# Kernel tuning notes

Measured on AMD Instinct MI355X. Metric: run time of the kernel, lower is better.

The kernel has to match this reference:

```python
import jax, jax.numpy as jnp
import numpy as np

WS = 7       # window_size
NH = 4       # num_head = dim_in // dim_head
HD = 64      # dim_head
ALPHA = 0.1
BETA = 0.2
THETA = 0.5
EPS = 1e-5   # LayerNorm eps


def dwconv(x, w):
    # x: [b, C, h, w], w: [C, 1, k, k] depthwise, padding 'same', no bias
    return jax.lax.conv_general_dilated(
        x, w, window_strides=(1, 1), padding='SAME',
        feature_group_count=x.shape[1],
        dimension_numbers=('NCHW', 'OIHW', 'NCHW'))


def setup_inputs() -> dict:
    key = jax.random.key(0)
    ks = jax.random.split(key, 8)
    B, H, W, C = 32, 56, 56, 256
    s = 0.02
    return {
        'x': jax.random.normal(ks[0], (B, H, W, C), jnp.float32),
        'qkv_w': jax.random.normal(ks[1], (3 * C, C), jnp.float32) * s,
        'qkv_b': jnp.zeros((3 * C,), jnp.float32),
        'conv3_w': jax.random.normal(ks[2], (C, 1, 3, 3), jnp.float32) * s,
        'conv5_w': jax.random.normal(ks[3], (C, 1, 5, 5), jnp.float32) * s,
        'conv7_w': jax.random.normal(ks[4], (C, 1, 7, 7), jnp.float32) * s,
        'ffn_in_w': jax.random.normal(ks[5], (C, C), jnp.float32) * s,
        'ffn_out_w': jax.random.normal(ks[6], (C, C), jnp.float32) * s,
        'ln_g': jnp.ones((C,), jnp.float32),
        'ln_b': jnp.zeros((C,), jnp.float32),
    }


def reference(x, qkv_w, qkv_b, conv3_w, conv5_w, conv7_w, ffn_in_w, ffn_out_w, ln_g, ln_b):
    B, H, W, C = x.shape
    n1, n2 = H // WS, W // WS  # H,W divisible by WS -> no padding path
    # rearrange 'b (h1 n1) (w1 n2) c -> (b n1 n2) h1 w1 c' (window dim is MAJOR axis)
    xw = x.reshape(B, WS, n1, WS, n2, C).transpose(0, 2, 4, 1, 3, 5)
    xw = xw.reshape(B * n1 * n2, WS, WS, C)
    b, hw = B * n1 * n2, WS * WS

    shortcut = xw.reshape(b, hw, NH, HD).transpose(0, 2, 1, 3)  # [b, nh, hw, hd]
    qkv = xw.reshape(b, hw, C) @ qkv_w.T + qkv_b                # [b, hw, 3C]
    qkv = qkv.reshape(b, hw, 3, NH, HD).transpose(2, 0, 3, 1, 4)
    q, k, v = qkv[0], qkv[1], qkv[2]
    v = ALPHA * v + shortcut                                     # scaled residual into V
    shortcut2 = v.transpose(0, 2, 1, 3).reshape(b, WS, WS, C)    # [b, h, w, C]

    # SDPA with default scale hd^-0.5
    attn = jax.nn.softmax(jnp.einsum('bnqd,bnkd->bnqk', q, k) * (HD ** -0.5), axis=-1)
    x_spa = jnp.einsum('bnqk,bnkd->bnqd', attn, v)
    x_spa = x_spa.transpose(0, 2, 1, 3).reshape(b, WS, WS, C)

    # conv branches on modified v: v.transpose(-1,-2).reshape(b, C, h, w)
    xc = v.transpose(0, 1, 3, 2).reshape(b, C, WS, WS)
    c3 = dwconv(xc, conv3_w).transpose(0, 2, 3, 1)
    c5 = dwconv(xc, conv5_w).transpose(0, 2, 3, 1)
    c7 = dwconv(xc, conv7_w).transpose(0, 2, 3, 1)
    x_spa = 0.25 * (x_spa + c3 + c5 + c7)  # equal 0.25 branch weights

    xw = BETA * x_spa + shortcut2
    # inverse rearrange '(b n1 n2) h1 w1 c -> b (h1 n1) (w1 n2) c'
    xo = xw.reshape(B, n1, n2, WS, WS, C).transpose(0, 3, 1, 4, 2, 5).reshape(B, H, W, C)

    # FFN (bias=False) with scaled residual, then LayerNorm
    y = jax.nn.silu(xo @ ffn_in_w.T) @ ffn_out_w.T
    xo = THETA * y + xo
    mu = jnp.mean(xo, axis=-1, keepdims=True)
    var = jnp.var(xo, axis=-1, keepdims=True)
    return (xo - mu) / jnp.sqrt(var + EPS) * ln_g + ln_b
```

## Files before the change

### kernel.cpp

```cpp
#include <hip/hip_runtime.h>

typedef unsigned short u16;
typedef unsigned short u16x8 __attribute__((ext_vector_type(8)));
typedef unsigned short u16x4 __attribute__((ext_vector_type(4)));
typedef unsigned int   u32x2 __attribute__((ext_vector_type(2)));
typedef short          s16x8 __attribute__((ext_vector_type(8)));
typedef float          f32x4 __attribute__((ext_vector_type(4)));

#define DEV static __device__ __forceinline__

DEV float bf2f(u16 u){ unsigned int v = ((unsigned int)u) << 16; return __builtin_bit_cast(float, v); }
DEV u16 f2bf(float f){
  unsigned int u = __builtin_bit_cast(unsigned int, f);
  u += 0x7fffu + ((u >> 16) & 1u);
  return (u16)(u >> 16);
}

DEV f32x4 mfma16(u16x8 a, u16x8 b, f32x4 c){
  return __builtin_amdgcn_mfma_f32_16x16x32_bf16(
      __builtin_bit_cast(s16x8, a), __builtin_bit_cast(s16x8, b), c, 0, 0, 0);
}

DEV void g2l16(const void* g, void* l){
  __builtin_amdgcn_global_load_lds((const __attribute__((address_space(1))) void*)g,
                                   (__attribute__((address_space(3))) void*)l, 16, 0, 0);
}

DEV size_t xrow_from(int b, int hw){
  int h1 = hw / 7, w1 = hw - h1 * 7;
  return ((size_t)(((b >> 6) * 56 + h1 * 8 + ((b >> 3) & 7)) * 56 + (w1 * 8 + (b & 7)))) << 8;
}
DEV size_t xrow_off(int t){ int b = t / 49; return xrow_from(b, t - b * 49); }

__global__ __launch_bounds__(256) void k_prep(const float* __restrict__ qkvw,
                                              const float* __restrict__ c3,
                                              const float* __restrict__ c5,
                                              const float* __restrict__ c7,
                                              const float* __restrict__ fin,
                                              const float* __restrict__ fout,
                                              u16* __restrict__ wq, u16* __restrict__ wfi,
                                              u16* __restrict__ wfo, float* __restrict__ weffT){
  int id = blockIdx.x * 256 + threadIdx.x;
  if (id < 196608) { wq[id] = f2bf(qkvw[id]); return; }
  id -= 196608;
  if (id < 65536) { wfi[id] = f2bf(fin[id]); return; }
  id -= 65536;
  if (id < 65536) { wfo[id] = f2bf(fout[id]); return; }
  id -= 65536;
  if (id < 12544) {
    int c = id / 49, t = id - c * 49;
    int di = t / 7 - 3, dj = t % 7 - 3;
    float s = c7[c * 49 + t];
    if (di >= -2 && di <= 2 && dj >= -2 && dj <= 2) s += c5[c * 25 + (di + 2) * 5 + (dj + 2)];
    if (di >= -1 && di <= 1 && dj >= -1 && dj <= 1) s += c3[c * 9 + (di + 1) * 3 + (dj + 1)];
    weffT[c * 52 + t] = 0.05f * s;
  }
}

__global__ __launch_bounds__(256) void k_xbf(const float* __restrict__ x, u16* __restrict__ xbf){
  int tid = threadIdx.x;
  int tok = blockIdx.x * 4 + (tid >> 6);
  int c4 = (tid & 63) * 4;
  float4 v = *(const float4*)(x + xrow_off(tok) + c4);
  u16x4 o; o[0] = f2bf(v.x); o[1] = f2bf(v.y); o[2] = f2bf(v.z); o[3] = f2bf(v.w);
  *(u16x4*)&xbf[(size_t)tok * 256 + c4] = o;
}

__global__ __launch_bounds__(256) void k_qkv(const u16* __restrict__ xbf,
                                             const u16* __restrict__ wq,
                                             const float* __restrict__ qkvb,
                                             u16* __restrict__ qb, u16* __restrict__ kb,
                                             u16* __restrict__ vmb){
  __shared__ __align__(16) u16 As[128 * 64];
  __shared__ __align__(16) u16 Bs[128 * 64];
  const int bid = blockIdx.x;
  const int lin = (bid & 7) * 588 + (bid >> 3);
  const int bm = lin / 6, bn = lin - bm * 6;
  const int tid = threadIdx.x, lane = tid & 63, wid = tid >> 6;
  const int wm = wid >> 1, wn = wid & 1;
  const int r = lane & 15, g = lane >> 4;
  const int lr = lane >> 3;
  const int swz = ((lane & 7) ^ lr) * 16;
  const f32x4 fz = {0.f, 0.f, 0.f, 0.f};
  f32x4 acc[4][4];
#pragma unroll
  for (int m = 0; m < 4; ++m)
#pragma unroll
    for (int n = 0; n < 4; ++n) acc[m][n] = fz;

  const char* gA0 = (const char*)xbf + (size_t)bm * 128 * 512;
  const char* gB0 = (const char*)wq  + (size_t)bn * 128 * 512;

  for (int kt = 0; kt < 4; ++kt) {
#pragma unroll
    for (int ri = 0; ri < 4; ++ri) {
      int chunk = ri * 4 + wid;
      int row = chunk * 8 + lr;
      g2l16(gA0 + (size_t)row * 512 + kt * 128 + swz, (char*)As + chunk * 1024);
      g2l16(gB0 + (size_t)row * 512 + kt * 128 + swz, (char*)Bs + chunk * 1024);
    }
    __syncthreads();
#pragma unroll
    for (int kk = 0; kk < 2; ++kk) {
      u16x8 af[4], bq[4];
#pragma unroll
      for (int m = 0; m < 4; ++m)
        af[m] = *(const u16x8*)&As[(wm * 64 + m * 16 + r) * 64 + (((kk * 4 + g) ^ (r & 7)) * 8)];
#pragma unroll
      for (int n = 0; n < 4; ++n)
        bq[n] = *(const u16x8*)&Bs[(wn * 64 + n * 16 + r) * 64 + (((kk * 4 + g) ^ (r & 7)) * 8)];
#pragma unroll
      for (int m = 0; m < 4; ++m)
#pragma unroll
        for (int n = 0; n < 4; ++n) acc[m][n] = mfma16(af[m], bq[n], acc[m][n]);
    }
    __syncthreads();
  }

  const int sec = bn >> 1;
  const int cb = (bn & 1) * 128 + wn * 64;
  u16* const outp = (sec == 0) ? qb : (sec == 1) ? kb : vmb;
  float bias[4];
#pragma unroll
  for (int n = 0; n < 4; ++n) bias[n] = qkvb[sec * 256 + cb + n * 16 + r];
#pragma unroll
  for (int m = 0; m < 4; ++m) {
#pragma unroll
    for (int i = 0; i < 4; ++i) {
      int t = bm * 128 + wm * 64 + m * 16 + g * 4 + i;
      u16* dst = outp + (size_t)t * 256 + cb;
      if (sec == 0) {
#pragma unroll
        for (int n = 0; n < 4; ++n) dst[n * 16 + r] = f2bf((acc[m][n][i] + bias[n]) * 0.125f);
      } else if (sec == 1) {
#pragma unroll
        for (int n = 0; n < 4; ++n) dst[n * 16 + r] = f2bf(acc[m][n][i] + bias[n]);
      } else {
        const u16* xsrc = xbf + (size_t)t * 256 + cb;
#pragma unroll
        for (int n = 0; n < 4; ++n)
          dst[n * 16 + r] = f2bf(0.1f * (acc[m][n][i] + bias[n]) + bf2f(xsrc[n * 16 + r]));
      }
    }
  }
}

template<int HW0, int NPIX>
DEV void conv_do(const float (&in_f)[49], const float (&wreg)[49], const u16* xs,
                 int c, size_t obase, u16* __restrict__ xo){
#pragma unroll
  for (int p = 0; p < NPIX; ++p) {
    const int hw = HW0 + p;
    const int i0 = hw / 7, j0 = hw % 7;
    float a = 0.f;
#pragma unroll
    for (int di = -3; di <= 3; ++di) {
      const int ii = i0 + di;
      if (ii < 0 || ii > 6) continue;
#pragma unroll
      for (int dj = -3; dj <= 3; ++dj) {
        const int jj = j0 + dj;
        if (jj < 0 || jj > 6) continue;
        a += in_f[ii * 7 + jj] * wreg[(di + 3) * 7 + (dj + 3)];
      }
    }
    float xsv = bf2f(xs[hw * 72 + c]);
    float outv = in_f[hw] + 0.05f * xsv + a;
    xo[obase + (size_t)hw * 256] = f2bf(outv);
  }
}

__global__ __launch_bounds__(256) void k_attn(const u16* __restrict__ qb,
                                              const u16* __restrict__ kb,
                                              const u16* __restrict__ vmb,
                                              const float* __restrict__ weffT,
                                              u16* __restrict__ xo){
  __shared__ __align__(16) u16 smem[18432];
  const int bx = blockIdx.x;
  const int b = bx >> 1, hp = bx & 1;
  const int tid = threadIdx.x, lane = tid & 63, wid = tid >> 6;
  const int hl = wid >> 1, hf = wid & 1;
  const int hg = hp * 2 + hl;
  const int vto = hl * 9216, po = hl * 9216 + 4608;
  const int r = lane & 15, g = lane >> 4;
  const size_t tok0 = (size_t)b * 49;
  const int hc = hg * 64;

  if (hf == 0) {
    int c = lane;
    u16 pix[49];
#pragma unroll
    for (int hw = 0; hw < 49; ++hw) pix[hw] = vmb[(tok0 + hw) * 256 + hc + c];
#pragma unroll
    for (int t2 = 0; t2 < 12; ++t2) {
      u32x2 w;
      w[0] = (unsigned)pix[4 * t2] | ((unsigned)pix[4 * t2 + 1] << 16);
      w[1] = (unsigned)pix[4 * t2 + 2] | ((unsigned)pix[4 * t2 + 3] << 16);
      *(u32x2*)&smem[vto + c * 72 + 4 * t2] = w;
    }
    u32x2 wl; wl[0] = (unsigned)pix[48]; wl[1] = 0u;
    *(u32x2*)&smem[vto + c * 72 + 48] = wl;
    u32x2 z; z[0] = 0u; z[1] = 0u;
    *(u32x2*)&smem[vto + c * 72 + 52] = z;
    *(u32x2*)&smem[vto + c * 72 + 56] = z;
    *(u32x2*)&smem[vto + c * 72 + 60] = z;
  }

  const int mt0 = hf * 2;
  const f32x4 fz = {0.f, 0.f, 0.f, 0.f};
  f32x4 s[2][4];
#pragma unroll
  for (int m = 0; m < 2; ++m)
#pragma unroll
    for (int n = 0; n < 4; ++n) s[m][n] = fz;
  u16x8 aq[2][2], bk[4][2];
#pragma unroll
  for (int m = 0; m < 2; ++m) {
    int qrow = (mt0 + m) * 16 + r; if (qrow > 48) qrow = 48;
    const u16* src = qb + (tok0 + qrow) * 256 + hc;
    aq[m][0] = *(const u16x8*)(src + g * 8);
    aq[m][1] = *(const u16x8*)(src + 32 + g * 8);
  }
#pragma unroll
  for (int n = 0; n < 4; ++n) {
    int krow = n * 16 + r; if (krow > 48) krow = 0;
    const u16* src = kb + (tok0 + krow) * 256 + hc;
    bk[n][0] = *(const u16x8*)(src + g * 8);
    bk[n][1] = *(const u16x8*)(src + 32 + g * 8);
  }
#pragma unroll
  for (int kk = 0; kk < 2; ++kk)
#pragma unroll
    for (int m = 0; m < 2; ++m)
#pragma unroll
      for (int n = 0; n < 4; ++n) s[m][n] = mfma16(aq[m][kk], bk[n][kk], s[m][n]);

#pragma unroll
  for (int m = 0; m < 2; ++m) {
#pragma unroll
    for (int i = 0; i < 4; ++i) {
      float x0 = s[m][0][i], x1 = s[m][1][i], x2 = s[m][2][i];
      float x3 = (r >= 1) ? -1e30f : s[m][3][i];
      float mx = fmaxf(fmaxf(x0, x1), fmaxf(x2, x3));
#pragma unroll
      for (int off = 1; off < 16; off <<= 1) mx = fmaxf(mx, __shfl_xor(mx, off, 64));
      float e0 = __expf(x0 - mx), e1 = __expf(x1 - mx), e2 = __expf(x2 - mx);
      float e3 = (r >= 1) ? 0.f : __expf(x3 - mx);
      float sum = e0 + e1 + e2 + e3;
#pragma unroll
      for (int off = 1; off < 16; off <<= 1) sum += __shfl_xor(sum, off, 64);
      float inv = 1.f / sum;
      int rowp = po + ((mt0 + m) * 16 + g * 4 + i) * 72;
      smem[rowp + r]       = f2bf(e0 * inv);
      smem[rowp + 16 + r]  = f2bf(e1 * inv);
      smem[rowp + 32 + r]  = f2bf(e2 * inv);
      smem[rowp + 48 + r]  = f2bf(e3 * inv);
    }
  }
  __syncthreads();

  f32x4 o[2][4];
#pragma unroll
  for (int m = 0; m < 2; ++m)
#pragma unroll
    for (int n = 0; n < 4; ++n) o[m][n] = fz;
#pragma unroll
  for (int kk = 0; kk < 2; ++kk) {
    u16x8 pa[2], vb[4];
#pragma unroll
    for (int m = 0; m < 2; ++m) pa[m] = *(const u16x8*)&smem[po + ((mt0 + m) * 16 + r) * 72 + kk * 32 + g * 8];
#pragma unroll
    for (int n = 0; n < 4; ++n) vb[n] = *(const u16x8*)&smem[vto + (n * 16 + r) * 72 + kk * 32 + g * 8];
#pragma unroll
    for (int m = 0; m < 2; ++m)
#pragma unroll
      for (int n = 0; n < 4; ++n) o[m][n] = mfma16(pa[m], vb[n], o[m][n]);
  }
#pragma unroll
  for (int m = 0; m < 2; ++m)
#pragma unroll
    for (int n = 0; n < 4; ++n)
#pragma unroll
      for (int i = 0; i < 4; ++i)
        smem[po + ((mt0 + m) * 16 + g * 4 + i) * 72 + n * 16 + r] = f2bf(o[m][n][i]);
  __syncthreads();

  {
    int c = lane;
    float in_f[49];
#pragma unroll
    for (int t2 = 0; t2 < 6; ++t2) {
      u16x8 raw = *(const u16x8*)&smem[vto + c * 72 + t2 * 8];
#pragma unroll
      for (int e = 0; e < 8; ++e) in_f[t2 * 8 + e] = bf2f(raw[e]);
    }
    in_f[48] = bf2f(smem[vto + c * 72 + 48]);
    float wreg[49];
    const float* wsrc = weffT + (size_t)(hc + c) * 52;
#pragma unroll
    for (int j = 0; j < 12; ++j) {
      float4 v = *(const float4*)(wsrc + j * 4);
      wreg[j * 4] = v.x; wreg[j * 4 + 1] = v.y; wreg[j * 4 + 2] = v.z; wreg[j * 4 + 3] = v.w;
    }
    wreg[48] = wsrc[48];
    size_t obase = tok0 * 256 + hc + c;
    if (hf == 0) conv_do<0, 25>(in_f, wreg, &smem[po], c, obase, xo);
    else         conv_do<25, 24>(in_f, wreg, &smem[po], c, obase, xo);
  }
}

__global__ __launch_bounds__(256) void k_ffn1(const u16* __restrict__ xo,
                                              const u16* __restrict__ wfi,
                                              u16* __restrict__ h){
  __shared__ __align__(16) u16 As[128 * 64];
  __shared__ __align__(16) u16 Bs[128 * 64];
  const int bid = blockIdx.x;
  const int lin = (bid & 7) * 196 + (bid >> 3);
  const int bm = lin >> 1, bn = lin & 1;
  const int tid = threadIdx.x, lane = tid & 63, wid = tid >> 6;
  const int wm = wid >> 1, wn = wid & 1;
  const int r = lane & 15, g = lane >> 4;
  const int lr = lane >> 3;
  const int swz = ((lane & 7) ^ lr) * 16;
  const f32x4 fz = {0.f, 0.f, 0.f, 0.f};
  f32x4 acc[4][4];
#pragma unroll
  for (int m = 0; m < 4; ++m)
#pragma unroll
    for (int n = 0; n < 4; ++n) acc[m][n] = fz;

  const char* gA0 = (const char*)xo + (size_t)bm * 128 * 512;
  const char* gB0 = (const char*)wfi + (size_t)bn * 128 * 512;

  for (int kt = 0; kt < 4; ++kt) {
#pragma unroll
    for (int ri = 0; ri < 4; ++ri) {
      int chunk = ri * 4 + wid;
      int row = chunk * 8 + lr;
      g2l16(gA0 + (size_t)row * 512 + kt * 128 + swz, (char*)As + chunk * 1024);
      g2l16(gB0 + (size_t)row * 512 + kt * 128 + swz, (char*)Bs + chunk * 1024);
    }
    __syncthreads();
#pragma unroll
    for (int kk = 0; kk < 2; ++kk) {
      u16x8 af[4], bq[4];
#pragma unroll
      for (int m = 0; m < 4; ++m)
        af[m] = *(const u16x8*)&As[(wm * 64 + m * 16 + r) * 64 + (((kk * 4 + g) ^ (r & 7)) * 8)];
#pragma unroll
      for (int n = 0; n < 4; ++n)
        bq[n] = *(const u16x8*)&Bs[(wn * 64 + n * 16 + r) * 64 + (((kk * 4 + g) ^ (r & 7)) * 8)];
#pragma unroll
      for (int m = 0; m < 4; ++m)
#pragma unroll
        for (int n = 0; n < 4; ++n) acc[m][n] = mfma16(af[m], bq[n], acc[m][n]);
    }
    __syncthreads();
  }
#pragma unroll
  for (int m = 0; m < 4; ++m)
#pragma unroll
    for (int i = 0; i < 4; ++i) {
      int t = bm * 128 + wm * 64 + m * 16 + g * 4 + i;
      u16* dst = h + (size_t)t * 256 + bn * 128 + wn * 64;
#pragma unroll
      for (int n = 0; n < 4; ++n) {
        float v = acc[m][n][i];
        float sg = v / (1.f + __expf(-v));
        dst[n * 16 + r] = f2bf(sg);
      }
    }
}

__global__ __launch_bounds__(512) void k_ffn2(const u16* __restrict__ h,
                                              const u16* __restrict__ wfo,
                                              const u16* __restrict__ xo,
                                              const float* __restrict__ lng,
                                              const float* __restrict__ lnb,
                                              float* __restrict__ out){
  __shared__ __align__(16) u16 As[128 * 64];
  __shared__ __align__(16) u16 Bs[256 * 64];
  __shared__ float red1[4][128];
  __shared__ float red2[4][128];
  const int bm = blockIdx.x;
  const int tid = threadIdx.x, lane = tid & 63, wid = tid >> 6;
  const int wm = wid >> 2, wn = wid & 3;
  const int r = lane & 15, g = lane >> 4;
  const int lr = lane >> 3;
  const int swz = ((lane & 7) ^ lr) * 16;
  const f32x4 fz = {0.f, 0.f, 0.f, 0.f};
  f32x4 acc[4][4];
#pragma unroll
  for (int m = 0; m < 4; ++m)
#pragma unroll
    for (int n = 0; n < 4; ++n) acc[m][n] = fz;

  for (int kt = 0; kt < 4; ++kt) {
#pragma unroll
    for (int ri = 0; ri < 2; ++ri) {
      int chunk = ri * 8 + wid;
      int row = chunk * 8 + lr;
      g2l16((const char*)h + (size_t)(bm * 128 + row) * 512 + kt * 128 + swz, (char*)As + chunk * 1024);
    }
#pragma unroll
    for (int ri = 0; ri < 4; ++ri) {
      int chunk = ri * 8 + wid;
      int row = chunk * 8 + lr;
      g2l16((const char*)wfo + (size_t)row * 512 + kt * 128 + swz, (char*)Bs + chunk * 1024);
    }
    __syncthreads();
#pragma unroll
    for (int kk = 0; kk < 2; ++kk) {
      u16x8 af[4], bq[4];
#pragma unroll
      for (int m = 0; m < 4; ++m)
        af[m] = *(const u16x8*)&As[(wm * 64 + m * 16 + r) * 64 + (((kk * 4 + g) ^ (r & 7)) * 8)];
#pragma unroll
      for (int n = 0; n < 4; ++n)
        bq[n] = *(const u16x8*)&Bs[(wn * 64 + n * 16 + r) * 64 + (((kk * 4 + g) ^ (r & 7)) * 8)];
#pragma unroll
      for (int m = 0; m < 4; ++m)
#pragma unroll
        for (int n = 0; n < 4; ++n) acc[m][n] = mfma16(af[m], bq[n], acc[m][n]);
    }
    __syncthreads();
  }

  float lg[4], lb[4];
#pragma unroll
  for (int n = 0; n < 4; ++n) {
    int col = wn * 64 + n * 16 + r;
    lg[n] = lng[col]; lb[n] = lnb[col];
  }
#pragma unroll
  for (int m = 0; m < 4; ++m)
#pragma unroll
    for (int i = 0; i < 4; ++i) {
      int t = bm * 128 + wm * 64 + m * 16 + g * 4 + i;
      const u16* xsrc = xo + (size_t)t * 256;
#pragma unroll
      for (int n = 0; n < 4; ++n) {
        int col = wn * 64 + n * 16 + r;
        acc[m][n][i] = 0.5f * acc[m][n][i] + bf2f(xsrc[col]);
      }
    }
#pragma unroll
  for (int m = 0; m < 4; ++m)
#pragma unroll
    for (int i = 0; i < 4; ++i) {
      float s1 = 0.f, s2 = 0.f;
#pragma unroll
      for (int n = 0; n < 4; ++n) { float v = acc[m][n][i]; s1 += v; s2 += v * v; }
#pragma unroll
      for (int off = 1; off < 16; off <<= 1) { s1 += __shfl_xor(s1, off, 64); s2 += __shfl_xor(s2, off, 64); }
      if (r == 0) {
        int rl = wm * 64 + m * 16 + g * 4 + i;
        red1[wn][rl] = s1; red2[wn][rl] = s2;
      }
    }
  __syncthreads();
#pragma unroll
  for (int m = 0; m < 4; ++m)
#pragma unroll
    for (int i = 0; i < 4; ++i) {
      int rl = wm * 64 + m * 16 + g * 4 + i;
      float S1 = red1[0][rl] + red1[1][rl] + red1[2][rl] + red1[3][rl];
      float S2 = red2[0][rl] + red2[1][rl] + red2[2][rl] + red2[3][rl];
      float mu = S1 * (1.f / 256.f);
      float var = S2 * (1.f / 256.f) - mu * mu;
      float rstd = rsqrtf(var + 1e-5f);
      int t = bm * 128 + rl;
      int b49 = t / 49, hw = t - b49 * 49;
      size_t ob = xrow_from(b49, hw);
#pragma unroll
      for (int n = 0; n < 4; ++n) {
        int col = wn * 64 + n * 16 + r;
        out[ob + col] = (acc[m][n][i] - mu) * rstd * lg[n] + lb[n];
      }
    }
}

extern "C" void kernel_launch(void* const* d_in, const int* in_sizes, int n_in,
                              void* d_out, int out_size, void* d_ws, size_t ws_size,
                              hipStream_t stream) {
  (void)in_sizes; (void)n_in; (void)out_size; (void)ws_size;
  const float* x     = (const float*)d_in[0];
  const float* qkvw  = (const float*)d_in[1];
  const float* qkvb  = (const float*)d_in[2];
  const float* c3    = (const float*)d_in[3];
  const float* c5    = (const float*)d_in[4];
  const float* c7    = (const float*)d_in[5];
  const float* fin   = (const float*)d_in[6];
  const float* fout  = (const float*)d_in[7];
  const float* lng   = (const float*)d_in[8];
  const float* lnb   = (const float*)d_in[9];
  float* out = (float*)d_out;
  char* ws = (char*)d_ws;

  u16*   qbuf  = (u16*)(ws);
  u16*   kbuf  = (u16*)(ws + 51380224);
  u16*   vmb   = (u16*)(ws + 102760448);
  u16*   wq    = (u16*)(ws + 154140672);
  u16*   wfi   = (u16*)(ws + 154533888);
  u16*   wfo   = (u16*)(ws + 154664960);
  float* weffT = (float*)(ws + 154796032);
  u16*   xbf   = (u16*)d_out;

  k_prep<<<dim3(1329), dim3(256), 0, stream>>>(qkvw, c3, c5, c7, fin, fout, wq, wfi, wfo, weffT);
  k_xbf<<<dim3(25088), dim3(256), 0, stream>>>(x, xbf);
  k_qkv<<<dim3(4704), dim3(256), 0, stream>>>(xbf, wq, qkvb, qbuf, kbuf, vmb);
  k_attn<<<dim3(4096), dim3(256), 0, stream>>>(qbuf, kbuf, vmb, weffT, kbuf );
  k_ffn1<<<dim3(1568), dim3(256), 0, stream>>>(kbuf , wfi, qbuf );
  k_ffn2<<<dim3(784), dim3(512), 0, stream>>>(qbuf , wfo, kbuf , lng, lnb, out);
}
```

Baseline: 264.5 us.

## Fuse FFN1 and FFN2 into one kernel keeping SiLU hidden in LDS

Merges the two FFN GEMM kernels into a single 512-thread kernel. Each block computes a full 128x256 hidden tile, applies SiLU, stores it as bf16 in a padded LDS buffer, then runs the second GEMM reading A directly from LDS. This removes the global write and re-read of the hidden activation and one kernel launch. The cost is about 67KB more shared memory per block (lower occupancy), and the whole FFN1 output width is computed per block instead of being split across two blocks. Block indices are also remapped with an 8-way interleave.

```diff
diff --git a/kernel.cpp b/kernel.cpp
--- a/kernel.cpp
+++ b/kernel.cpp
@@ -309,80 +309,19 @@
   }
 }
 
-__global__ __launch_bounds__(256) void k_ffn1(const u16* __restrict__ xo,
-                                              const u16* __restrict__ wfi,
-                                              u16* __restrict__ h){
-  __shared__ __align__(16) u16 As[128 * 64];
-  __shared__ __align__(16) u16 Bs[128 * 64];
-  const int bid = blockIdx.x;
-  const int lin = (bid & 7) * 196 + (bid >> 3);
-  const int bm = lin >> 1, bn = lin & 1;
-  const int tid = threadIdx.x, lane = tid & 63, wid = tid >> 6;
-  const int wm = wid >> 1, wn = wid & 1;
-  const int r = lane & 15, g = lane >> 4;
-  const int lr = lane >> 3;
-  const int swz = ((lane & 7) ^ lr) * 16;
-  const f32x4 fz = {0.f, 0.f, 0.f, 0.f};
-  f32x4 acc[4][4];
-#pragma unroll
-  for (int m = 0; m < 4; ++m)
-#pragma unroll
-    for (int n = 0; n < 4; ++n) acc[m][n] = fz;
-
-  const char* gA0 = (const char*)xo + (size_t)bm * 128 * 512;
-  const char* gB0 = (const char*)wfi + (size_t)bn * 128 * 512;
-
-  for (int kt = 0; kt < 4; ++kt) {
-#pragma unroll
-    for (int ri = 0; ri < 4; ++ri) {
-      int chunk = ri * 4 + wid;
-      int row = chunk * 8 + lr;
-      g2l16(gA0 + (size_t)row * 512 + kt * 128 + swz, (char*)As + chunk * 1024);
-      g2l16(gB0 + (size_t)row * 512 + kt * 128 + swz, (char*)Bs + chunk * 1024);
-    }
-    __syncthreads();
-#pragma unroll
-    for (int kk = 0; kk < 2; ++kk) {
-      u16x8 af[4], bq[4];
-#pragma unroll
-      for (int m = 0; m < 4; ++m)
-        af[m] = *(const u16x8*)&As[(wm * 64 + m * 16 + r) * 64 + (((kk * 4 + g) ^ (r & 7)) * 8)];
-#pragma unroll
-      for (int n = 0; n < 4; ++n)
-        bq[n] = *(const u16x8*)&Bs[(wn * 64 + n * 16 + r) * 64 + (((kk * 4 + g) ^ (r & 7)) * 8)];
-#pragma unroll
-      for (int m = 0; m < 4; ++m)
-#pragma unroll
-        for (int n = 0; n < 4; ++n) acc[m][n] = mfma16(af[m], bq[n], acc[m][n]);
-    }
-    __syncthreads();
-  }
-#pragma unroll
-  for (int m = 0; m < 4; ++m)
-#pragma unroll
-    for (int i = 0; i < 4; ++i) {
-      int t = bm * 128 + wm * 64 + m * 16 + g * 4 + i;
-      u16* dst = h + (size_t)t * 256 + bn * 128 + wn * 64;
-#pragma unroll
-      for (int n = 0; n < 4; ++n) {
-        float v = acc[m][n][i];
-        float sg = v / (1.f + __expf(-v));
-        dst[n * 16 + r] = f2bf(sg);
-      }
-    }
-}
-
-__global__ __launch_bounds__(512) void k_ffn2(const u16* __restrict__ h,
-                                              const u16* __restrict__ wfo,
-                                              const u16* __restrict__ xo,
-                                              const float* __restrict__ lng,
-                                              const float* __restrict__ lnb,
-                                              float* __restrict__ out){
+__global__ __launch_bounds__(512) void k_ffn(const u16* __restrict__ xo,
+                                             const u16* __restrict__ wfi,
+                                             const u16* __restrict__ wfo,
+                                             const float* __restrict__ lng,
+                                             const float* __restrict__ lnb,
+                                             float* __restrict__ out){
   __shared__ __align__(16) u16 As[128 * 64];
   __shared__ __align__(16) u16 Bs[256 * 64];
+  __shared__ __align__(16) u16 hs[128 * 264];
   __shared__ float red1[4][128];
   __shared__ float red2[4][128];
-  const int bm = blockIdx.x;
+  const int bid = blockIdx.x;
+  const int bm = (bid & 7) * 98 + (bid >> 3);
   const int tid = threadIdx.x, lane = tid & 63, wid = tid >> 6;
   const int wm = wid >> 2, wn = wid & 3;
   const int r = lane & 15, g = lane >> 4;
@@ -395,13 +334,57 @@
 #pragma unroll
     for (int n = 0; n < 4; ++n) acc[m][n] = fz;
 
+  const char* gA0 = (const char*)xo + (size_t)bm * 128 * 512;
+
   for (int kt = 0; kt < 4; ++kt) {
 #pragma unroll
     for (int ri = 0; ri < 2; ++ri) {
       int chunk = ri * 8 + wid;
       int row = chunk * 8 + lr;
-      g2l16((const char*)h + (size_t)(bm * 128 + row) * 512 + kt * 128 + swz, (char*)As + chunk * 1024);
-    }
+      g2l16(gA0 + (size_t)row * 512 + kt * 128 + swz, (char*)As + chunk * 1024);
+    }
+#pragma unroll
+    for (int ri = 0; ri < 4; ++ri) {
+      int chunk = ri * 8 + wid;
+      int row = chunk * 8 + lr;
+      g2l16((const char*)wfi + (size_t)row * 512 + kt * 128 + swz, (char*)Bs + chunk * 1024);
+    }
+    __syncthreads();
+#pragma unroll
+    for (int kk = 0; kk < 2; ++kk) {
+      u16x8 af[4], bq[4];
+#pragma unroll
+      for (int m = 0; m < 4; ++m)
+        af[m] = *(const u16x8*)&As[(wm * 64 + m * 16 + r) * 64 + (((kk * 4 + g) ^ (r & 7)) * 8)];
+#pragma unroll
+      for (int n = 0; n < 4; ++n)
+        bq[n] = *(const u16x8*)&Bs[(wn * 64 + n * 16 + r) * 64 + (((kk * 4 + g) ^ (r & 7)) * 8)];
+#pragma unroll
+      for (int m = 0; m < 4; ++m)
+#pragma unroll
+        for (int n = 0; n < 4; ++n) acc[m][n] = mfma16(af[m], bq[n], acc[m][n]);
+    }
+    __syncthreads();
+  }
+#pragma unroll
+  for (int m = 0; m < 4; ++m)
+#pragma unroll
+    for (int i = 0; i < 4; ++i) {
+      int row = wm * 64 + m * 16 + g * 4 + i;
+#pragma unroll
+      for (int n = 0; n < 4; ++n) {
+        int col = wn * 64 + n * 16 + r;
+        float v = acc[m][n][i];
+        hs[row * 264 + col] = f2bf(v / (1.f + __expf(-v)));
+      }
+    }
+  __syncthreads();
+
+#pragma unroll
+  for (int m = 0; m < 4; ++m)
+#pragma unroll
+    for (int n = 0; n < 4; ++n) acc[m][n] = fz;
+  for (int kt = 0; kt < 4; ++kt) {
 #pragma unroll
     for (int ri = 0; ri < 4; ++ri) {
       int chunk = ri * 8 + wid;
@@ -414,7 +397,7 @@
       u16x8 af[4], bq[4];
 #pragma unroll
       for (int m = 0; m < 4; ++m)
-        af[m] = *(const u16x8*)&As[(wm * 64 + m * 16 + r) * 64 + (((kk * 4 + g) ^ (r & 7)) * 8)];
+        af[m] = *(const u16x8*)&hs[(wm * 64 + m * 16 + r) * 264 + kt * 64 + kk * 32 + g * 8];
 #pragma unroll
       for (int n = 0; n < 4; ++n)
         bq[n] = *(const u16x8*)&Bs[(wn * 64 + n * 16 + r) * 64 + (((kk * 4 + g) ^ (r & 7)) * 8)];
@@ -510,6 +493,5 @@
   k_xbf<<<dim3(25088), dim3(256), 0, stream>>>(x, xbf);
   k_qkv<<<dim3(4704), dim3(256), 0, stream>>>(xbf, wq, qkvb, qbuf, kbuf, vmb);
   k_attn<<<dim3(4096), dim3(256), 0, stream>>>(qbuf, kbuf, vmb, weffT, kbuf );
-  k_ffn1<<<dim3(1568), dim3(256), 0, stream>>>(kbuf , wfi, qbuf );
-  k_ffn2<<<dim3(784), dim3(512), 0, stream>>>(qbuf , wfo, kbuf , lng, lnb, out);
-}
+  k_ffn<<<dim3(784), dim3(512), 0, stream>>>(kbuf , wfi, wfo, lng, lnb, out);
+}
```

Measured after the change: 268.7 us. Within noise of the previous version (+1.6%).
